# Performance work log

Measured on AMD Instinct MI355X. Metric: run time of the kernel, lower is better.

## Reference

```python
import math
import jax, jax.numpy as jnp
import numpy as np

NUM_HEADS = 16

def _rotate_half(t):
    t1, t2 = jnp.split(t, 2, axis=-1)
    return jnp.concatenate([-t2, t1], axis=-1)

def _apply_rope(t, cos, sin):
    # t: [B, H, S, D]; cos/sin: [S, D] broadcast over batch and heads
    c = cos[None, None, :, :]
    s = sin[None, None, :, :]
    return t * c + _rotate_half(t) * s

def setup_inputs() -> dict:
    key = jax.random.key(0)
    k1, k2, k3, k4, k5 = jax.random.split(key, 5)
    B, S, E, D = 4, 2048, 1024, 1024 // NUM_HEADS
    x = jax.random.normal(k1, (B, S, E), dtype=jnp.float32)
    cos = jax.random.uniform(k2, (S, D), dtype=jnp.float32)
    sin = jax.random.uniform(k3, (S, D), dtype=jnp.float32)
    W_qkv = jax.random.normal(k4, (3 * E, E), dtype=jnp.float32) * (1.0 / math.sqrt(E))
    W_out = jax.random.normal(k5, (E, E), dtype=jnp.float32) * (1.0 / math.sqrt(E))
    return {"x": x, "cos": cos, "sin": sin, "W_qkv": W_qkv, "W_out": W_out}

def reference(x, cos, sin, W_qkv, W_out):
    B, S, E = x.shape
    H = NUM_HEADS
    D = E // H
    # fused QKV projection (torch Linear: y = x @ W^T)
    qkv = jnp.einsum('bse,fe->bsf', x, W_qkv)
    qkv = qkv.reshape(B, S, 3, H, D).transpose(2, 0, 3, 1, 4)  # [3, B, H, S, D]
    q, k, v = qkv[0], qkv[1], qkv[2]
    q = _apply_rope(q, cos, sin)
    k = _apply_rope(k, cos, sin)
    # naive fp32 attention: full [B,H,S,S] score matrix, stable softmax
    scale = 1.0 / math.sqrt(D)
    qf = q.astype(jnp.float32)
    kf = k.astype(jnp.float32)
    vf = v.astype(jnp.float32)
    scores = jnp.einsum('bhqd,bhkd->bhqk', qf, kf) * scale
    attn = jax.nn.softmax(scores, axis=-1)
    o = jnp.einsum('bhqk,bhkd->bhqd', attn, vf).astype(x.dtype)
    o = o.transpose(0, 2, 1, 3).reshape(B, S, E)
    return jnp.einsum('bse,fe->bsf', o, W_out)
```

## Files before the change

### kernel.cpp

```cpp
#include <hip/hip_runtime.h>
#include <hip/hip_bf16.h>

using bf16 = __hip_bfloat16;
typedef __attribute__((ext_vector_type(4))) float f32x4;
typedef __attribute__((ext_vector_type(16))) float f32x16;
typedef short s16x8 __attribute__((ext_vector_type(8)));
typedef unsigned short u16x8 __attribute__((ext_vector_type(8)));

__device__ __forceinline__ unsigned short f2b(float f) {
  bf16 h = __float2bfloat16(f);
  return __builtin_bit_cast(unsigned short, h);
}
__device__ __forceinline__ unsigned cvt_pk_bf16(float lo, float hi) {
  unsigned r;
  asm volatile("v_cvt_pk_bf16_f32 %0, %1, %2" : "=v"(r) : "v"(lo), "v"(hi));
  return r;
}
__device__ __forceinline__ void pl32_swap(unsigned& a, unsigned& b) {
  asm volatile("v_permlane32_swap_b32 %0, %1" : "+v"(a), "+v"(b));
}
__device__ __forceinline__ float fast_exp2(float x) {
#if __has_builtin(__builtin_amdgcn_exp2f)
  return __builtin_amdgcn_exp2f(x);
#else
  return exp2f(x);
#endif
}

__device__ __forceinline__ void async_copy16(const void* g, void* lds) {
  __builtin_amdgcn_global_load_lds(
      (const __attribute__((address_space(1))) void*)g,
      (__attribute__((address_space(3))) void*)lds, 16, 0, 0);
}

__global__ __launch_bounds__(256) void cvt_all(const float* __restrict__ x,
                                               const float* __restrict__ wqkv,
                                               const float* __restrict__ wout,
                                               ushort* __restrict__ out) {
  long c = (long)blockIdx.x * 256 + threadIdx.x;
  const float* src;
  long off;
  if (c < 1048576)      { src = x;    off = c; }
  else if (c < 1441792) { src = wqkv; off = c - 1048576; }
  else                  { src = wout; off = c - 1441792; }
  float4 a = *(const float4*)(src + off * 8);
  float4 b = *(const float4*)(src + off * 8 + 4);
  u16x8 o;
  o[0] = f2b(a.x); o[1] = f2b(a.y); o[2] = f2b(a.z); o[3] = f2b(a.w);
  o[4] = f2b(b.x); o[5] = f2b(b.y); o[6] = f2b(b.z); o[7] = f2b(b.w);
  *(u16x8*)(out + c * 8) = o;
}

__global__ __launch_bounds__(256) void transpose_v(const bf16* __restrict__ qkv,
                                                   ushort* __restrict__ vtg) {
  const int pair = blockIdx.y;
  const int b = pair >> 4, h = pair & 15;
  const int st = blockIdx.x * 64;
  const int tid = threadIdx.x;
  __shared__ ushort T[64][68];
  const ushort* src = (const ushort*)qkv + (long)(b * 2048 + st) * 3072 + 2048 + h * 64;
#pragma unroll
  for (int i = 0; i < 4; ++i) {
    int c2 = tid + i * 256;
    int row = c2 >> 4;
    int d4 = (c2 & 15) * 4;
    *(ushort4*)&T[row][d4] = *(const ushort4*)(src + (long)row * 3072 + d4);
  }
  __syncthreads();
#pragma unroll
  for (int i = 0; i < 4; ++i) {
    int c2 = tid + i * 256;
    int d = c2 >> 4;
    int s4 = (c2 & 15) * 4;
    ushort4 w;
    w.x = T[s4][d]; w.y = T[s4 + 1][d]; w.z = T[s4 + 2][d]; w.w = T[s4 + 3][d];
    *(ushort4*)(vtg + (long)pair * 131072 + (long)d * 2048 + st + s4) = w;
  }
}

__device__ __forceinline__ void storeC(float* p, float v) { *p = v; }
__device__ __forceinline__ void storeC(bf16* p, float v) { *p = __float2bfloat16(v); }

template <typename CT, bool ROPE>
__global__ __launch_bounds__(256) void gemm_bt(const bf16* __restrict__ A,
                                               const bf16* __restrict__ B,
                                               CT* __restrict__ C,
                                               int M, int N, int K,
                                               const float* __restrict__ cosT,
                                               const float* __restrict__ sinT) {
  __shared__ bf16 As[2][128 * 64];
  __shared__ bf16 Bs[2][128 * 64];
  const int tid = threadIdx.x;
  const int lane = tid & 63;
  const int wid = tid >> 6;

  const int nwg = gridDim.x * gridDim.y;
  const int orig = blockIdx.y * gridDim.x + blockIdx.x;
  const int wgid = (orig & 7) * (nwg >> 3) + (orig >> 3);
  const int bx = wgid % gridDim.x;
  const int by = wgid / gridDim.x;

  const int tm = by * 128;
  const int tn = bx * 128;
  const int wr = wid >> 1, wc = wid & 1;
  const int srow = tid >> 3;
  const int scolb = (tid & 7) * 16;
  const int sscolb = scolb ^ ((srow & 7) << 4);

  f32x4 acc[4][4] = {};

  const bf16* Abase = A + (long)(tm + srow) * K + (sscolb >> 1);
  const bf16* Bbase = B + (long)(tn + srow) * K + (sscolb >> 1);

  const int lr = lane & 15;
  const int g = lane >> 4;
  const int sw = (lr & 7) << 4;

  auto stage = [&](int k0, int bb) {
#pragma unroll
    for (int i = 0; i < 4; ++i) {
      async_copy16(Abase + (long)i * 32 * K + k0, (char*)As[bb] + wid * 1024 + i * 4096);
      async_copy16(Bbase + (long)i * 32 * K + k0, (char*)Bs[bb] + wid * 1024 + i * 4096);
    }
  };

  const int nk = K >> 6;
  stage(0, 0);
  stage(64, 1);

  for (int kt = 0; kt < nk; ++kt) {
    const int cur = kt & 1;
    if (kt + 1 < nk) asm volatile("s_waitcnt vmcnt(8)" ::: "memory");
    else             asm volatile("s_waitcnt vmcnt(0)" ::: "memory");
    __builtin_amdgcn_s_barrier();
    __builtin_amdgcn_sched_barrier(0);

#pragma unroll
    for (int ks = 0; ks < 2; ++ks) {
      s16x8 af[4], bff[4];
#pragma unroll
      for (int m = 0; m < 4; ++m) {
        int row = wr * 64 + m * 16 + lr;
        af[m] = *(const s16x8*)((const char*)&As[cur][0] + row * 128 +
                                ((ks * 64 + g * 16) ^ sw));
      }
#pragma unroll
      for (int n = 0; n < 4; ++n) {
        int row = wc * 64 + n * 16 + lr;
        bff[n] = *(const s16x8*)((const char*)&Bs[cur][0] + row * 128 +
                                 ((ks * 64 + g * 16) ^ sw));
      }
#pragma unroll
      for (int m = 0; m < 4; ++m)
#pragma unroll
        for (int n = 0; n < 4; ++n)
          acc[m][n] = __builtin_amdgcn_mfma_f32_16x16x32_bf16(af[m], bff[n], acc[m][n], 0, 0, 0);
    }

    __builtin_amdgcn_s_barrier();
    __builtin_amdgcn_sched_barrier(0);
    if (kt + 2 < nk) stage((kt + 2) << 6, cur);
  }

  const int cc = lane & 15;
  const int cr = (lane >> 4) * 4;
  const int wcol = tn + wc * 64;

  if (ROPE && wcol < 2048) {
    const float sc = (wcol < 1024) ? 0.18033688011112042f : 1.0f;
#pragma unroll
    for (int m = 0; m < 4; ++m)
#pragma unroll
      for (int n = 0; n < 2; ++n) {
        long row0 = tm + wr * 64 + m * 16 + cr;
        long col = wcol + n * 16 + cc;
        int d = n * 16 + cc;
#pragma unroll
        for (int r = 0; r < 4; ++r) {
          int s = (int)((row0 + r) & 2047);
          float lo = acc[m][n][r], hi = acc[m][n + 2][r];
          float c0 = cosT[s * 64 + d], s0v = sinT[s * 64 + d];
          float c1 = cosT[s * 64 + d + 32], s1v = sinT[s * 64 + d + 32];
          storeC(&C[(row0 + r) * (long)N + col], (lo * c0 - hi * s0v) * sc);
          storeC(&C[(row0 + r) * (long)N + col + 32], (hi * c1 + lo * s1v) * sc);
        }
      }
  } else {
#pragma unroll
    for (int m = 0; m < 4; ++m)
#pragma unroll
      for (int n = 0; n < 4; ++n) {
        long row0 = tm + wr * 64 + m * 16 + cr;
        long col = wcol + n * 16 + cc;
#pragma unroll
        for (int r = 0; r < 4; ++r)
          storeC(&C[(row0 + r) * (long)N + col], acc[m][n][r]);
      }
  }
}

__global__ __launch_bounds__(256, 4) void attn_kernel(const bf16* __restrict__ qkv,
                                                      const ushort* __restrict__ vtg,
                                                      ushort* __restrict__ o) {
  const int bid = blockIdx.x;
  const int xcd = bid & 7;
  const int w = bid >> 3;
  const int pair = xcd * 8 + (w >> 4);
  const int qtile = w & 15;
  const int b = pair >> 4, h = pair & 15;
  const int q0 = qtile * 128;
  const int tid = threadIdx.x, lane = tid & 63, wid = tid >> 6;

  const bf16* Qb = qkv + (long)b * 2048 * 3072 + h * 64;
  const bf16* Kb = Qb + 1024;
  const ushort* Vg = vtg + (long)pair * 131072;

  __shared__ bf16 Ks[2][64 * 64];
  __shared__ bf16 Vs[2][64 * 64];

  const int ql = lane & 31;
  const int hi = lane >> 5;
  const int sw = (ql & 7) << 4;

  s16x8 qa[4];
  {
    const bf16* qrow = Qb + (long)(q0 + wid * 32 + ql) * 3072 + hi * 8;
#pragma unroll
    for (int ds = 0; ds < 4; ++ds)
      qa[ds] = *(const s16x8*)(qrow + ds * 16);
  }

  f32x16 oacc[2] = {};
  float lrow = 0.f;

  auto stage = [&](int kt, int bb) {
#pragma unroll
    for (int i = 0; i < 2; ++i) {
      int c = tid + i * 256;
      int row = c >> 3;
      int colb = (c & 7) * 16;
      int scolb = colb ^ ((row & 7) << 4);
      async_copy16(Kb + (long)(kt * 64 + row) * 3072 + (scolb >> 1),
                   (char*)Ks + bb * 8192 + wid * 1024 + i * 4096);
      async_copy16(Vg + (long)row * 2048 + kt * 64 + (scolb >> 1),
                   (char*)Vs + bb * 8192 + wid * 1024 + i * 4096);
    }
  };

  stage(0, 0);
  __syncthreads();

  int cur = 0;
  for (int kt = 0; kt < 32; ++kt) {
    if (kt < 31) stage(kt + 1, cur ^ 1);

    f32x16 sacc[2] = {};
    __builtin_amdgcn_s_setprio(1);
#pragma unroll
    for (int kb = 0; kb < 2; ++kb) {
      const char* krow = (const char*)Ks + cur * 8192 + (kb * 32 + ql) * 128;
#pragma unroll
      for (int ds = 0; ds < 4; ++ds) {
        s16x8 kf = *(const s16x8*)(krow + ((ds * 32 + hi * 16) ^ sw));
        sacc[kb] = __builtin_amdgcn_mfma_f32_32x32x16_bf16(kf, qa[ds], sacc[kb], 0, 0, 0);
      }
    }
    __builtin_amdgcn_s_setprio(0);

    float pv[32];
#pragma unroll
    for (int r = 0; r < 16; ++r) {
      pv[r] = fast_exp2(sacc[0][r]);
      pv[16 + r] = fast_exp2(sacc[1][r]);
    }
    float s16a[16];
#pragma unroll
    for (int i = 0; i < 16; ++i) s16a[i] = pv[i] + pv[i + 16];
#pragma unroll
    for (int i = 0; i < 8; ++i) s16a[i] += s16a[i + 8];
#pragma unroll
    for (int i = 0; i < 4; ++i) s16a[i] += s16a[i + 4];
    float psum = (s16a[0] + s16a[1]) + (s16a[2] + s16a[3]);
    psum += __shfl_xor(psum, 32, 64);
    lrow += psum;

    s16x8 pa[4];
#pragma unroll
    for (int s = 0; s < 4; ++s) {
      unsigned a0 = cvt_pk_bf16(pv[s * 8 + 0], pv[s * 8 + 1]);
      unsigned a1 = cvt_pk_bf16(pv[s * 8 + 2], pv[s * 8 + 3]);
      unsigned b0 = cvt_pk_bf16(pv[s * 8 + 4], pv[s * 8 + 5]);
      unsigned b1 = cvt_pk_bf16(pv[s * 8 + 6], pv[s * 8 + 7]);
      pl32_swap(a0, b0);
      pl32_swap(a1, b1);
      uint4 u{a0, a1, b0, b1};
      pa[s] = __builtin_bit_cast(s16x8, u);
    }

    __builtin_amdgcn_s_setprio(1);
#pragma unroll
    for (int dblk = 0; dblk < 2; ++dblk) {
      const char* vrow = (const char*)Vs + cur * 8192 + (dblk * 32 + ql) * 128;
#pragma unroll
      for (int s = 0; s < 4; ++s) {
        s16x8 vf = *(const s16x8*)(vrow + ((s * 32 + hi * 16) ^ sw));
        oacc[dblk] = __builtin_amdgcn_mfma_f32_32x32x16_bf16(pa[s], vf, oacc[dblk], 0, 0, 0);
      }
    }
    __builtin_amdgcn_s_setprio(0);

    __syncthreads();
    cur ^= 1;
  }

  float linv = 1.f / lrow;
#pragma unroll
  for (int r = 0; r < 16; ++r) {
    int qr = (r & 3) + 8 * (r >> 2) + 4 * hi;
    float inv = __shfl(linv, qr, 64);
    long srow = q0 + wid * 32 + qr;
    ushort* orow = o + ((long)b * 2048 + srow) * 1024 + h * 64 + ql;
    orow[0]  = f2b(oacc[0][r] * inv);
    orow[32] = f2b(oacc[1][r] * inv);
  }
}

extern "C" void kernel_launch(void* const* d_in, const int* in_sizes, int n_in,
                              void* d_out, int out_size, void* d_ws, size_t ws_size,
                              hipStream_t stream) {
  const float* x    = (const float*)d_in[0];
  const float* cosT = (const float*)d_in[1];
  const float* sinT = (const float*)d_in[2];
  const float* Wqkv = (const float*)d_in[3];
  const float* Wout = (const float*)d_in[4];
  float* out = (float*)d_out;

  char* p = (char*)d_ws;
  bf16* xb    = (bf16*)p; p += (size_t)8192 * 1024 * 2;
  bf16* wqkvb = (bf16*)p; p += (size_t)3072 * 1024 * 2;
  bf16* woutb = (bf16*)p; p += (size_t)1024 * 1024 * 2;
  bf16* qkvb  = (bf16*)p; p += (size_t)8192 * 3072 * 2;
  bf16* ob    = (bf16*)p;
  ushort* vtg = (ushort*)xb;

  cvt_all<<<6144, 256, 0, stream>>>(x, Wqkv, Wout, (ushort*)xb);

  gemm_bt<bf16, true><<<dim3(24, 64), 256, 0, stream>>>(xb, wqkvb, qkvb, 8192, 3072, 1024,
                                                        cosT, sinT);

  transpose_v<<<dim3(32, 64), 256, 0, stream>>>(qkvb, vtg);

  attn_kernel<<<1024, 256, 0, stream>>>(qkvb, vtg, (ushort*)ob);

  gemm_bt<float, false><<<dim3(8, 64), 256, 0, stream>>>(ob, woutb, out, 8192, 1024, 1024,
                                                         nullptr, nullptr);
}
```

Before: 181.1 us.

## Process two 32-row query blocks per wave in attention to reuse K/V fragments

Each wave now handles 64 query rows as two 32-row sub-blocks, so the attention tile per block doubles to 256 queries and the grid halves to 512 blocks. K fragments are loaded from LDS once per key tile and reused for both sub-blocks, and each V fragment feeds two MFMAs, which halves LDS reads and global K/V staging per query. The cost is more registers (launch bounds drop from 4 to 2 blocks per CU), fewer blocks to fill the GPU, and lower occupancy for hiding latency.

```diff
diff --git a/kernel.cpp b/kernel.cpp
--- a/kernel.cpp
+++ b/kernel.cpp
@@ -199,16 +199,16 @@
   }
 }
 
-__global__ __launch_bounds__(256, 4) void attn_kernel(const bf16* __restrict__ qkv,
+__global__ __launch_bounds__(256, 2) void attn_kernel(const bf16* __restrict__ qkv,
                                                       const ushort* __restrict__ vtg,
                                                       ushort* __restrict__ o) {
   const int bid = blockIdx.x;
   const int xcd = bid & 7;
   const int w = bid >> 3;
-  const int pair = xcd * 8 + (w >> 4);
-  const int qtile = w & 15;
+  const int pair = xcd * 8 + (w >> 3);
+  const int qtile = w & 7;
   const int b = pair >> 4, h = pair & 15;
-  const int q0 = qtile * 128;
+  const int q0 = qtile * 256;
   const int tid = threadIdx.x, lane = tid & 63, wid = tid >> 6;
 
   const bf16* Qb = qkv + (long)b * 2048 * 3072 + h * 64;
@@ -222,16 +222,17 @@
   const int hi = lane >> 5;
   const int sw = (ql & 7) << 4;
 
-  s16x8 qa[4];
-  {
-    const bf16* qrow = Qb + (long)(q0 + wid * 32 + ql) * 3072 + hi * 8;
+  s16x8 qa[2][4];
+#pragma unroll
+  for (int m = 0; m < 2; ++m) {
+    const bf16* qrow = Qb + (long)(q0 + wid * 64 + m * 32 + ql) * 3072 + hi * 8;
 #pragma unroll
     for (int ds = 0; ds < 4; ++ds)
-      qa[ds] = *(const s16x8*)(qrow + ds * 16);
-  }
-
-  f32x16 oacc[2] = {};
-  float lrow = 0.f;
+      qa[m][ds] = *(const s16x8*)(qrow + ds * 16);
+  }
+
+  f32x16 oacc[2][2] = {};
+  float lrow[2] = {0.f, 0.f};
 
   auto stage = [&](int kt, int bb) {
 #pragma unroll
@@ -254,47 +255,56 @@
   for (int kt = 0; kt < 32; ++kt) {
     if (kt < 31) stage(kt + 1, cur ^ 1);
 
-    f32x16 sacc[2] = {};
-    __builtin_amdgcn_s_setprio(1);
+    s16x8 kf[8];
 #pragma unroll
     for (int kb = 0; kb < 2; ++kb) {
       const char* krow = (const char*)Ks + cur * 8192 + (kb * 32 + ql) * 128;
 #pragma unroll
-      for (int ds = 0; ds < 4; ++ds) {
-        s16x8 kf = *(const s16x8*)(krow + ((ds * 32 + hi * 16) ^ sw));
-        sacc[kb] = __builtin_amdgcn_mfma_f32_32x32x16_bf16(kf, qa[ds], sacc[kb], 0, 0, 0);
-      }
-    }
-    __builtin_amdgcn_s_setprio(0);
-
-    float pv[32];
-#pragma unroll
-    for (int r = 0; r < 16; ++r) {
-      pv[r] = fast_exp2(sacc[0][r]);
-      pv[16 + r] = fast_exp2(sacc[1][r]);
-    }
-    float s16a[16];
-#pragma unroll
-    for (int i = 0; i < 16; ++i) s16a[i] = pv[i] + pv[i + 16];
-#pragma unroll
-    for (int i = 0; i < 8; ++i) s16a[i] += s16a[i + 8];
-#pragma unroll
-    for (int i = 0; i < 4; ++i) s16a[i] += s16a[i + 4];
-    float psum = (s16a[0] + s16a[1]) + (s16a[2] + s16a[3]);
-    psum += __shfl_xor(psum, 32, 64);
-    lrow += psum;
-
-    s16x8 pa[4];
-#pragma unroll
-    for (int s = 0; s < 4; ++s) {
-      unsigned a0 = cvt_pk_bf16(pv[s * 8 + 0], pv[s * 8 + 1]);
-      unsigned a1 = cvt_pk_bf16(pv[s * 8 + 2], pv[s * 8 + 3]);
-      unsigned b0 = cvt_pk_bf16(pv[s * 8 + 4], pv[s * 8 + 5]);
-      unsigned b1 = cvt_pk_bf16(pv[s * 8 + 6], pv[s * 8 + 7]);
-      pl32_swap(a0, b0);
-      pl32_swap(a1, b1);
-      uint4 u{a0, a1, b0, b1};
-      pa[s] = __builtin_bit_cast(s16x8, u);
+      for (int ds = 0; ds < 4; ++ds)
+        kf[kb * 4 + ds] = *(const s16x8*)(krow + ((ds * 32 + hi * 16) ^ sw));
+    }
+
+    s16x8 pa[2][4];
+#pragma unroll
+    for (int m = 0; m < 2; ++m) {
+      f32x16 sacc[2] = {};
+      __builtin_amdgcn_s_setprio(1);
+#pragma unroll
+      for (int kb = 0; kb < 2; ++kb)
+#pragma unroll
+        for (int ds = 0; ds < 4; ++ds)
+          sacc[kb] = __builtin_amdgcn_mfma_f32_32x32x16_bf16(kf[kb * 4 + ds], qa[m][ds],
+                                                             sacc[kb], 0, 0, 0);
+      __builtin_amdgcn_s_setprio(0);
+
+      float pv[32];
+#pragma unroll
+      for (int r = 0; r < 16; ++r) {
+        pv[r] = fast_exp2(sacc[0][r]);
+        pv[16 + r] = fast_exp2(sacc[1][r]);
+      }
+      float s16a[16];
+#pragma unroll
+      for (int i = 0; i < 16; ++i) s16a[i] = pv[i] + pv[i + 16];
+#pragma unroll
+      for (int i = 0; i < 8; ++i) s16a[i] += s16a[i + 8];
+#pragma unroll
+      for (int i = 0; i < 4; ++i) s16a[i] += s16a[i + 4];
+      float psum = (s16a[0] + s16a[1]) + (s16a[2] + s16a[3]);
+      psum += __shfl_xor(psum, 32, 64);
+      lrow[m] += psum;
+
+#pragma unroll
+      for (int s = 0; s < 4; ++s) {
+        unsigned a0 = cvt_pk_bf16(pv[s * 8 + 0], pv[s * 8 + 1]);
+        unsigned a1 = cvt_pk_bf16(pv[s * 8 + 2], pv[s * 8 + 3]);
+        unsigned b0 = cvt_pk_bf16(pv[s * 8 + 4], pv[s * 8 + 5]);
+        unsigned b1 = cvt_pk_bf16(pv[s * 8 + 6], pv[s * 8 + 7]);
+        pl32_swap(a0, b0);
+        pl32_swap(a1, b1);
+        uint4 u{a0, a1, b0, b1};
+        pa[m][s] = __builtin_bit_cast(s16x8, u);
+      }
     }
 
     __builtin_amdgcn_s_setprio(1);
@@ -304,7 +314,8 @@
 #pragma unroll
       for (int s = 0; s < 4; ++s) {
         s16x8 vf = *(const s16x8*)(vrow + ((s * 32 + hi * 16) ^ sw));
-        oacc[dblk] = __builtin_amdgcn_mfma_f32_32x32x16_bf16(pa[s], vf, oacc[dblk], 0, 0, 0);
+        oacc[0][dblk] = __builtin_amdgcn_mfma_f32_32x32x16_bf16(pa[0][s], vf, oacc[0][dblk], 0, 0, 0);
+        oacc[1][dblk] = __builtin_amdgcn_mfma_f32_32x32x16_bf16(pa[1][s], vf, oacc[1][dblk], 0, 0, 0);
       }
     }
     __builtin_amdgcn_s_setprio(0);
@@ -313,15 +324,18 @@
     cur ^= 1;
   }
 
-  float linv = 1.f / lrow;
-#pragma unroll
-  for (int r = 0; r < 16; ++r) {
-    int qr = (r & 3) + 8 * (r >> 2) + 4 * hi;
-    float inv = __shfl(linv, qr, 64);
-    long srow = q0 + wid * 32 + qr;
-    ushort* orow = o + ((long)b * 2048 + srow) * 1024 + h * 64 + ql;
-    orow[0]  = f2b(oacc[0][r] * inv);
-    orow[32] = f2b(oacc[1][r] * inv);
+#pragma unroll
+  for (int m = 0; m < 2; ++m) {
+    float linv = 1.f / lrow[m];
+#pragma unroll
+    for (int r = 0; r < 16; ++r) {
+      int qr = (r & 3) + 8 * (r >> 2) + 4 * hi;
+      float inv = __shfl(linv, qr, 64);
+      long srow = q0 + wid * 64 + m * 32 + qr;
+      ushort* orow = o + ((long)b * 2048 + srow) * 1024 + h * 64 + ql;
+      orow[0]  = f2b(oacc[m][0][r] * inv);
+      orow[32] = f2b(oacc[m][1][r] * inv);
+    }
   }
 }
 
@@ -350,7 +364,7 @@
 
   transpose_v<<<dim3(32, 64), 256, 0, stream>>>(qkvb, vtg);
 
-  attn_kernel<<<1024, 256, 0, stream>>>(qkvb, vtg, (ushort*)ob);
+  attn_kernel<<<512, 256, 0, stream>>>(qkvb, vtg, (ushort*)ob);
 
   gemm_bt<float, false><<<dim3(8, 64), 256, 0, stream>>>(ob, woutb, out, 8192, 1024, 1024,
                                                          nullptr, nullptr);
```

New measurement: 181.9 us. About the same (+0.4%).
